# Optimization experiments

Hardware: AMD Instinct MI355X
Metric: run time of the kernel (lower is better)

## Reference

```python
import jax, jax.numpy as jnp
import numpy as np

N, D, C = 4096, 512, 64
MARGIN = 1.0
INF = jnp.float32(1e30)


def setup_inputs() -> dict:
    key = jax.random.key(0)
    k1, k2 = jax.random.split(key)
    embeddings = jax.random.normal(k1, (N, D), dtype=jnp.float32)
    targets = jax.random.randint(k2, (N,), 0, C)
    return {"embeddings": embeddings, "targets": targets}


def _triplet_loss(embeddings, targets, margin=MARGIN):
    # Squared pairwise distances [N, N] (differentiable, used for the loss)
    sq_norms = jnp.sum(embeddings * embeddings, axis=1)
    sq_dist = jnp.maximum(
        sq_norms[:, None] + sq_norms[None, :] - 2.0 * (embeddings @ embeddings.T), 0.0
    )
    # Euclidean distances for mining only (index selection is non-differentiable in torch)
    dist = jnp.sqrt(jax.lax.stop_gradient(sq_dist))

    same = targets[:, None] == targets[None, :]  # [N, N] same-label mask

    # Hardest negative per anchor: argmax_k (d_ap - d_ak + margin) == argmin_k d_ak over negatives
    neg_dist = jnp.where(same, INF, dist)
    n_idx = jnp.argmin(neg_dist, axis=1)   # [N] hardest negative index per anchor
    min_neg = jnp.min(neg_dist, axis=1)    # [N] its euclidean distance

    idx = jnp.arange(dist.shape[0])
    # anchor-positive pairs: same label, a < p (torch.combinations on sorted indices)
    pair_mask = same & (idx[:, None] < idx[None, :])
    # triplet kept only if mined loss (euclidean) strictly positive
    valid = pair_mask & (dist - min_neg[:, None] + margin > 0)

    ap_sq = sq_dist                         # [N, N] squared anchor-positive distances
    an_sq = sq_dist[idx, n_idx]             # [N]   squared anchor-hard-negative distances
    losses = jax.nn.relu(ap_sq - an_sq[:, None] + margin)

    cnt = jnp.sum(valid)
    denom = jnp.maximum(cnt, 1).astype(losses.dtype)
    loss = jnp.sum(jnp.where(valid, losses, 0.0)) / denom

    correct = jnp.sum(valid & (ap_sq < an_sq[:, None]))
    accuracy = correct.astype(jnp.float32) / jnp.maximum(cnt, 1).astype(jnp.float32)
    return loss, accuracy


def reference(embeddings, targets):
    return _triplet_loss(embeddings, targets)
```

## Files before the change

### kernel.cpp

```cpp
#include <hip/hip_runtime.h>

#define N 4096
#define D 512
#define C 64
#define MARGIN 1.0f
#define TILE 128
#define ROWB 128
#define NTILES (N / TILE)
#define NTRI (NTILES * (NTILES + 1) / 2)
#define FINF 3.0e38f
#define MAXM 112
#define SKB 144
#define SLOTW 16
#define LOSS_G 7

typedef __attribute__((ext_vector_type(8))) short short8;
typedef __attribute__((ext_vector_type(4))) float floatx4;

__device__ __forceinline__ unsigned short f2bf(float f) {
  unsigned int u = __float_as_uint(f);
  u += 0x7FFFu + ((u >> 16) & 1u);
  return (unsigned short)(u >> 16);
}

__device__ __forceinline__ void gload_lds16(const void* g, void* l) {
  __builtin_amdgcn_global_load_lds(
      (const __attribute__((address_space(1))) unsigned int*)g,
      (__attribute__((address_space(3))) unsigned int*)l, 16, 0, 0);
}

__global__ __launch_bounds__(256) void prep_kernel(const float* __restrict__ E,
                                                   const int* __restrict__ targets,
                                                   unsigned short* __restrict__ Ebf,
                                                   float* __restrict__ norms,
                                                   unsigned int* __restrict__ an_sq_bits,
                                                   int* __restrict__ cls_mem,
                                                   int* __restrict__ cls_off,
                                                   unsigned int* __restrict__ accs_u,
                                                   unsigned int* __restrict__ done) {
  const int row = blockIdx.x;
  const int tid = threadIdx.x;
  if (row == N) {
    __shared__ unsigned int cnt[C];
    __shared__ unsigned int base[C];
    if (tid == 0) *done = 0u;
    for (int k = tid; k < C * SLOTW; k += 256) accs_u[k] = 0u;
    if (tid < C) cnt[tid] = 0;
    __syncthreads();
    for (int i = tid; i < N; i += 256) atomicAdd(&cnt[targets[i]], 1);
    __syncthreads();
    if (tid == 0) {
      unsigned int s = 0;
      for (int c = 0; c < C; c++) { base[c] = s; s += cnt[c]; }
    }
    __syncthreads();
    if (tid < C) cnt[tid] = base[tid];
    __syncthreads();
    for (int i = tid; i < N; i += 256) {
      const int c = targets[i];
      const unsigned int p = atomicAdd(&cnt[c], 1);
      cls_mem[p] = i;
    }
    if (tid < C) cls_off[tid] = (int)base[tid];
    if (tid == 0) cls_off[C] = N;
    return;
  }
  if (row < 16) an_sq_bits[row * 256 + tid] = 0x7F800000u;
  const float2 v = reinterpret_cast<const float2*>(E + (size_t)row * D)[tid];
  float s = v.x * v.x + v.y * v.y;
  unsigned int packed = ((unsigned int)f2bf(v.y) << 16) | (unsigned int)f2bf(v.x);
  reinterpret_cast<unsigned int*>(Ebf + (size_t)row * D)[tid] = packed;
  for (int off = 32; off > 0; off >>= 1) s += __shfl_down(s, off);
  __shared__ float wsum[4];
  if ((tid & 63) == 0) wsum[tid >> 6] = s;
  __syncthreads();
  if (tid == 0) norms[row] = wsum[0] + wsum[1] + wsum[2] + wsum[3];
}

__global__ __launch_bounds__(256, 3) void gemm_min_kernel(const unsigned short* __restrict__ Ebf,
                                                          const float* __restrict__ norms,
                                                          const int* __restrict__ targets,
                                                          unsigned int* __restrict__ an_sq_bits) {
  const int u = blockIdx.x;
  int i = (int)((sqrtf(8.0f * (float)u + 1.0f) - 1.0f) * 0.5f);
  while ((i + 1) * (i + 2) / 2 <= u) ++i;
  while (i * (i + 1) / 2 > u) --i;
  const int tm = u - i * (i + 1) / 2;
  const int tn = i;

  __shared__ alignas(16) unsigned char As[TILE * ROWB];
  __shared__ alignas(16) unsigned char Bs[TILE * ROWB];
  __shared__ float s_rmin[2][TILE];
  __shared__ float s_cmin[2][TILE];

  const int tid = threadIdx.x;
  const int wave = tid >> 6, lane = tid & 63;
  const int quad = lane >> 4, l16 = lane & 15;
  const int wr = wave >> 1, wc = wave & 1;
  const int rowBase = tm * TILE, colBase = tn * TILE;

  const int lr = lane >> 3;
  const int lq = (lane & 7) ^ lr;
  const int lofs = lr * (D * 2) + lq * 16;
  const unsigned char* gA = (const unsigned char*)Ebf + (size_t)rowBase * (D * 2);
  const unsigned char* gB = (const unsigned char*)Ebf + (size_t)colBase * (D * 2);

  const int swz = l16 & 7;
  int rA[4], rB[4], cq[2];
#pragma unroll
  for (int s = 0; s < 4; s++) {
    rA[s] = (wr * 64 + s * 16 + l16) * ROWB;
    rB[s] = (wc * 64 + s * 16 + l16) * ROWB;
  }
#pragma unroll
  for (int ks = 0; ks < 2; ks++) cq[ks] = ((ks * 4 + quad) ^ swz) * 16;

  floatx4 acc[4][4];
#pragma unroll
  for (int a = 0; a < 4; a++)
#pragma unroll
    for (int b = 0; b < 4; b++) acc[a][b] = (floatx4){0.f, 0.f, 0.f, 0.f};

  for (int k0b = 0; k0b < D * 2; k0b += 128) {
#pragma unroll
    for (int t = 0; t < 4; t++) {
      const int g = wave * 4 + t;
      gload_lds16(gA + (size_t)g * 8 * (D * 2) + lofs + k0b, As + g * 1024);
      gload_lds16(gB + (size_t)g * 8 * (D * 2) + lofs + k0b, Bs + g * 1024);
    }
    __syncthreads();
#pragma unroll
    for (int ks = 0; ks < 2; ks++) {
      short8 af[4], bf[4];
#pragma unroll
      for (int s = 0; s < 4; s++) {
        af[s] = *reinterpret_cast<const short8*>(As + rA[s] + cq[ks]);
        bf[s] = *reinterpret_cast<const short8*>(Bs + rB[s] + cq[ks]);
      }
#pragma unroll
      for (int sm = 0; sm < 4; sm++)
#pragma unroll
        for (int sn = 0; sn < 4; sn++)
          acc[sm][sn] = __builtin_amdgcn_mfma_f32_16x16x32_bf16(af[sm], bf[sn], acc[sm][sn], 0, 0, 0);
    }
    __syncthreads();
  }

  int tcol[4];
  float ncol[4];
#pragma unroll
  for (int sn = 0; sn < 4; sn++) {
    const int gc = colBase + wc * 64 + sn * 16 + l16;
    tcol[sn] = targets[gc];
    ncol[sn] = norms[gc];
  }
  float colmin[4] = {FINF, FINF, FINF, FINF};
#pragma unroll
  for (int sm = 0; sm < 4; sm++) {
#pragma unroll
    for (int r = 0; r < 4; r++) {
      const int rloc = wr * 64 + sm * 16 + quad * 4 + r;
      const int grow = rowBase + rloc;
      const int trow = targets[grow];
      const float nrow = norms[grow];
      float rowmin = FINF;
#pragma unroll
      for (int sn = 0; sn < 4; sn++) {
        const float sq = fmaxf(nrow + ncol[sn] - 2.0f * acc[sm][sn][r], 0.0f);
        if (tcol[sn] != trow) {
          rowmin = fminf(rowmin, sq);
          colmin[sn] = fminf(colmin[sn], sq);
        }
      }
#pragma unroll
      for (int off = 1; off < 16; off <<= 1) rowmin = fminf(rowmin, __shfl_xor(rowmin, off));
      if (l16 == 0) s_rmin[wc][rloc] = rowmin;
    }
  }
#pragma unroll
  for (int sn = 0; sn < 4; sn++) {
    float cm = colmin[sn];
    cm = fminf(cm, __shfl_xor(cm, 16));
    cm = fminf(cm, __shfl_xor(cm, 32));
    if (quad == 0) s_cmin[wr][wc * 64 + sn * 16 + l16] = cm;
  }
  __syncthreads();
  if (tid < TILE) {
    const float m = fminf(s_rmin[0][tid], s_rmin[1][tid]);
    if (m < FINF) atomicMin(&an_sq_bits[rowBase + tid], __float_as_uint(m));
  } else {
    const int c = tid - TILE;
    const float m = fminf(s_cmin[0][c], s_cmin[1][c]);
    if (m < FINF) atomicMin(&an_sq_bits[colBase + c], __float_as_uint(m));
  }
}

__global__ __launch_bounds__(256) void loss_kernel(const unsigned short* __restrict__ Ebf,
                                                   const float* __restrict__ norms,
                                                   const unsigned int* __restrict__ an_sq_bits,
                                                   const int* __restrict__ cls_mem,
                                                   const int* __restrict__ cls_off,
                                                   float* __restrict__ accs,
                                                   unsigned int* __restrict__ done,
                                                   float* __restrict__ out) {
  const int c = blockIdx.x, g = blockIdx.y;
  const int tid = threadIdx.x, wave = tid >> 6, lane = tid & 63;
  const int quad = lane >> 4, l16 = lane & 15;
  const int o = cls_off[c];
  const int s_c = min(cls_off[c + 1] - o, MAXM);
  const int nt = (s_c + 15) >> 4;
  const int npairs = nt * (nt + 1) / 2;
  const bool active = (g * 4 < npairs);

  __shared__ alignas(16) unsigned char S[MAXM * SKB];
  __shared__ int l_mem[MAXM];
  __shared__ float l_norm[MAXM];
  __shared__ float l_an[MAXM];
  __shared__ float s_sum[4];
  __shared__ unsigned int s_cnt[4], s_cor[4];
  __shared__ int s_last;

  if (active) {
    if (tid < s_c) {
      const int m = cls_mem[o + tid];
      l_mem[tid] = m;
      l_norm[tid] = norms[m];
      l_an[tid] = __uint_as_float(an_sq_bits[m]);
    }
    __syncthreads();
    const int p = g * 4 + wave;
    const bool havep = p < npairs;
    int ti = 0, tj = 0;
    if (havep) {
      int pp = p, t = 0;
      while (pp >= nt - t) { pp -= nt - t; t++; }
      ti = t; tj = t + pp;
    }
    floatx4 pacc = (floatx4){0.f, 0.f, 0.f, 0.f};
    for (int k0 = 0; k0 < D; k0 += 64) {
      for (int s = tid; s < s_c * 8; s += 256) {
        const int r = s >> 3, q = s & 7;
        *reinterpret_cast<uint4*>(&S[r * SKB + q * 16]) =
            *reinterpret_cast<const uint4*>(&Ebf[(size_t)l_mem[r] * D + k0 + q * 8]);
      }
      __syncthreads();
      if (havep) {
#pragma unroll
        for (int ks = 0; ks < 2; ks++) {
          const short8 af = *reinterpret_cast<const short8*>(&S[(ti * 16 + l16) * SKB + ks * 64 + quad * 16]);
          const short8 bf = *reinterpret_cast<const short8*>(&S[(tj * 16 + l16) * SKB + ks * 64 + quad * 16]);
          pacc = __builtin_amdgcn_mfma_f32_16x16x32_bf16(af, bf, pacc, 0, 0, 0);
        }
      }
      __syncthreads();
    }

    float bsum = 0.f;
    unsigned int bcnt = 0, bcor = 0;
    if (havep) {
#pragma unroll
      for (int r = 0; r < 4; r++) {
        const int i_loc = ti * 16 + quad * 4 + r;
        const int j_loc = tj * 16 + l16;
        if (i_loc < s_c && j_loc < s_c && (ti < tj || i_loc < j_loc)) {
          const int oi = l_mem[i_loc], oj = l_mem[j_loc];
          const float sq = fmaxf(l_norm[i_loc] + l_norm[j_loc] - 2.0f * pacc[r], 0.0f);
          const float an = (oi < oj) ? l_an[i_loc] : l_an[j_loc];
          if (sqrtf(sq) - sqrtf(an) + MARGIN > 0.0f) {
            bcnt++;
            bsum += fmaxf(sq - an + MARGIN, 0.0f);
            if (sq < an) bcor++;
          }
        }
      }
    }
#pragma unroll
    for (int off = 32; off > 0; off >>= 1) {
      bsum += __shfl_down(bsum, off);
      bcnt += __shfl_down(bcnt, off);
      bcor += __shfl_down(bcor, off);
    }
    if (lane == 0) { s_sum[wave] = bsum; s_cnt[wave] = bcnt; s_cor[wave] = bcor; }
    __syncthreads();
    if (tid == 0) {
      float* slot = accs + (size_t)c * SLOTW;
      atomicAdd(&slot[0], s_sum[0] + s_sum[1] + s_sum[2] + s_sum[3]);
      atomicAdd((unsigned int*)&slot[1], s_cnt[0] + s_cnt[1] + s_cnt[2] + s_cnt[3]);
      atomicAdd((unsigned int*)&slot[2], s_cor[0] + s_cor[1] + s_cor[2] + s_cor[3]);
    }
  }
  __syncthreads();
  if (tid == 0) {
    __threadfence();
    s_last = (atomicAdd(done, 1u) == (unsigned)(C * LOSS_G) - 1u);
  }
  __syncthreads();
  if (s_last) {
    __threadfence();
    if (tid < C) {
      float sum = __uint_as_float(atomicAdd((unsigned int*)&accs[(size_t)tid * SLOTW + 0], 0u));
      unsigned int cnt = atomicAdd((unsigned int*)&accs[(size_t)tid * SLOTW + 1], 0u);
      unsigned int cor = atomicAdd((unsigned int*)&accs[(size_t)tid * SLOTW + 2], 0u);
#pragma unroll
      for (int off = 32; off > 0; off >>= 1) {
        sum += __shfl_down(sum, off);
        cnt += __shfl_down(cnt, off);
        cor += __shfl_down(cor, off);
      }
      if (tid == 0) {
        const float denom = (float)(cnt > 0u ? cnt : 1u);
        out[0] = sum / denom;
        out[1] = (float)cor / denom;
      }
    }
  }
}

extern "C" void kernel_launch(void* const* d_in, const int* in_sizes, int n_in,
                              void* d_out, int out_size, void* d_ws, size_t ws_size,
                              hipStream_t stream) {
  const float* E = (const float*)d_in[0];
  const int* targets = (const int*)d_in[1];
  float* out = (float*)d_out;
  char* ws = (char*)d_ws;
  size_t off = 0;
  unsigned short* Ebf = (unsigned short*)(ws + off); off += (size_t)N * D * 2;
  float* norms = (float*)(ws + off); off += (size_t)N * 4;
  unsigned int* an_sq = (unsigned int*)(ws + off); off += (size_t)N * 4;
  float* accs = (float*)(ws + off); off += (size_t)C * SLOTW * 4;
  int* cls_mem = (int*)(ws + off); off += (size_t)N * 4;
  int* cls_off = (int*)(ws + off); off += 512;
  unsigned int* done = (unsigned int*)(ws + off);

  prep_kernel<<<dim3(N + 1), dim3(256), 0, stream>>>(E, targets, Ebf, norms, an_sq, cls_mem,
                                                     cls_off, (unsigned int*)accs, done);
  gemm_min_kernel<<<dim3(NTRI), dim3(256), 0, stream>>>(Ebf, norms, targets, an_sq);
  loss_kernel<<<dim3(C, LOSS_G), dim3(256), 0, stream>>>(Ebf, norms, an_sq, cls_mem, cls_off,
                                                         accs, done, out);
}
```

Measured before the change: 102.9 us.

## Emit same-class pair distances from GEMM epilogue and drop per-class recompute

```diff
diff --git a/kernel.cpp b/kernel.cpp
--- a/kernel.cpp
+++ b/kernel.cpp
@@ -9,10 +9,9 @@
 #define NTILES (N / TILE)
 #define NTRI (NTILES * (NTILES + 1) / 2)
 #define FINF 3.0e38f
-#define MAXM 112
-#define SKB 144
 #define SLOTW 16
-#define LOSS_G 7
+#define PCAP 1024
+#define LOSSB 128
 
 typedef __attribute__((ext_vector_type(8))) short short8;
 typedef __attribute__((ext_vector_type(4))) float floatx4;
@@ -30,39 +29,16 @@
 }
 
 __global__ __launch_bounds__(256) void prep_kernel(const float* __restrict__ E,
-                                                   const int* __restrict__ targets,
                                                    unsigned short* __restrict__ Ebf,
                                                    float* __restrict__ norms,
                                                    unsigned int* __restrict__ an_sq_bits,
-                                                   int* __restrict__ cls_mem,
-                                                   int* __restrict__ cls_off,
                                                    unsigned int* __restrict__ accs_u,
-                                                   unsigned int* __restrict__ done) {
+                                                   unsigned int* __restrict__ ctrl) {
   const int row = blockIdx.x;
   const int tid = threadIdx.x;
   if (row == N) {
-    __shared__ unsigned int cnt[C];
-    __shared__ unsigned int base[C];
-    if (tid == 0) *done = 0u;
     for (int k = tid; k < C * SLOTW; k += 256) accs_u[k] = 0u;
-    if (tid < C) cnt[tid] = 0;
-    __syncthreads();
-    for (int i = tid; i < N; i += 256) atomicAdd(&cnt[targets[i]], 1);
-    __syncthreads();
-    if (tid == 0) {
-      unsigned int s = 0;
-      for (int c = 0; c < C; c++) { base[c] = s; s += cnt[c]; }
-    }
-    __syncthreads();
-    if (tid < C) cnt[tid] = base[tid];
-    __syncthreads();
-    for (int i = tid; i < N; i += 256) {
-      const int c = targets[i];
-      const unsigned int p = atomicAdd(&cnt[c], 1);
-      cls_mem[p] = i;
-    }
-    if (tid < C) cls_off[tid] = (int)base[tid];
-    if (tid == 0) cls_off[C] = N;
+    if (tid < 2) ctrl[tid] = 0u;
     return;
   }
   if (row < 16) an_sq_bits[row * 256 + tid] = 0x7F800000u;
@@ -80,7 +56,9 @@
 __global__ __launch_bounds__(256, 3) void gemm_min_kernel(const unsigned short* __restrict__ Ebf,
                                                           const float* __restrict__ norms,
                                                           const int* __restrict__ targets,
-                                                          unsigned int* __restrict__ an_sq_bits) {
+                                                          unsigned int* __restrict__ an_sq_bits,
+                                                          uint2* __restrict__ pairs,
+                                                          unsigned int* __restrict__ ctrl) {
   const int u = blockIdx.x;
   int i = (int)((sqrtf(8.0f * (float)u + 1.0f) - 1.0f) * 0.5f);
   while ((i + 1) * (i + 2) / 2 <= u) ++i;
@@ -92,12 +70,16 @@
   __shared__ alignas(16) unsigned char Bs[TILE * ROWB];
   __shared__ float s_rmin[2][TILE];
   __shared__ float s_cmin[2][TILE];
+  __shared__ unsigned int s_pkey[PCAP];
+  __shared__ float s_psq[PCAP];
+  __shared__ unsigned int s_pcnt, s_pbase;
 
   const int tid = threadIdx.x;
   const int wave = tid >> 6, lane = tid & 63;
   const int quad = lane >> 4, l16 = lane & 15;
   const int wr = wave >> 1, wc = wave & 1;
   const int rowBase = tm * TILE, colBase = tn * TILE;
+  if (tid == 0) s_pcnt = 0u;
 
   const int lr = lane >> 3;
   const int lq = (lane & 7) ^ lr;
@@ -146,11 +128,12 @@
     __syncthreads();
   }
 
-  int tcol[4];
+  int tcol[4], gcolv[4];
   float ncol[4];
 #pragma unroll
   for (int sn = 0; sn < 4; sn++) {
     const int gc = colBase + wc * 64 + sn * 16 + l16;
+    gcolv[sn] = gc;
     tcol[sn] = targets[gc];
     ncol[sn] = norms[gc];
   }
@@ -170,6 +153,16 @@
         if (tcol[sn] != trow) {
           rowmin = fminf(rowmin, sq);
           colmin[sn] = fminf(colmin[sn], sq);
+        } else if (grow < gcolv[sn]) {
+          const unsigned int idx = atomicAdd(&s_pcnt, 1u);
+          if (idx < PCAP) {
+            s_pkey[idx] = ((unsigned int)grow << 12) | (unsigned int)gcolv[sn];
+            s_psq[idx] = sq;
+          } else {
+            const unsigned int g = atomicAdd(&ctrl[0], 1u);
+            pairs[g] = make_uint2(((unsigned int)grow << 12) | (unsigned int)gcolv[sn],
+                                  __float_as_uint(sq));
+          }
         }
       }
 #pragma unroll
@@ -193,106 +186,51 @@
     const float m = fminf(s_cmin[0][c], s_cmin[1][c]);
     if (m < FINF) atomicMin(&an_sq_bits[colBase + c], __float_as_uint(m));
   }
-}
-
-__global__ __launch_bounds__(256) void loss_kernel(const unsigned short* __restrict__ Ebf,
-                                                   const float* __restrict__ norms,
+  const unsigned int npair = min(s_pcnt, (unsigned int)PCAP);
+  if (tid == 0) s_pbase = atomicAdd(&ctrl[0], npair);
+  __syncthreads();
+  for (unsigned int r = tid; r < npair; r += 256)
+    pairs[s_pbase + r] = make_uint2(s_pkey[r], __float_as_uint(s_psq[r]));
+}
+
+__global__ __launch_bounds__(256) void loss_kernel(const uint2* __restrict__ pairs,
                                                    const unsigned int* __restrict__ an_sq_bits,
-                                                   const int* __restrict__ cls_mem,
-                                                   const int* __restrict__ cls_off,
                                                    float* __restrict__ accs,
-                                                   unsigned int* __restrict__ done,
+                                                   unsigned int* __restrict__ ctrl,
                                                    float* __restrict__ out) {
-  const int c = blockIdx.x, g = blockIdx.y;
   const int tid = threadIdx.x, wave = tid >> 6, lane = tid & 63;
-  const int quad = lane >> 4, l16 = lane & 15;
-  const int o = cls_off[c];
-  const int s_c = min(cls_off[c + 1] - o, MAXM);
-  const int nt = (s_c + 15) >> 4;
-  const int npairs = nt * (nt + 1) / 2;
-  const bool active = (g * 4 < npairs);
-
-  __shared__ alignas(16) unsigned char S[MAXM * SKB];
-  __shared__ int l_mem[MAXM];
-  __shared__ float l_norm[MAXM];
-  __shared__ float l_an[MAXM];
+  const unsigned int M = ctrl[0];
   __shared__ float s_sum[4];
   __shared__ unsigned int s_cnt[4], s_cor[4];
   __shared__ int s_last;
-
-  if (active) {
-    if (tid < s_c) {
-      const int m = cls_mem[o + tid];
-      l_mem[tid] = m;
-      l_norm[tid] = norms[m];
-      l_an[tid] = __uint_as_float(an_sq_bits[m]);
-    }
-    __syncthreads();
-    const int p = g * 4 + wave;
-    const bool havep = p < npairs;
-    int ti = 0, tj = 0;
-    if (havep) {
-      int pp = p, t = 0;
-      while (pp >= nt - t) { pp -= nt - t; t++; }
-      ti = t; tj = t + pp;
-    }
-    floatx4 pacc = (floatx4){0.f, 0.f, 0.f, 0.f};
-    for (int k0 = 0; k0 < D; k0 += 64) {
-      for (int s = tid; s < s_c * 8; s += 256) {
-        const int r = s >> 3, q = s & 7;
-        *reinterpret_cast<uint4*>(&S[r * SKB + q * 16]) =
-            *reinterpret_cast<const uint4*>(&Ebf[(size_t)l_mem[r] * D + k0 + q * 8]);
-      }
-      __syncthreads();
-      if (havep) {
-#pragma unroll
-        for (int ks = 0; ks < 2; ks++) {
-          const short8 af = *reinterpret_cast<const short8*>(&S[(ti * 16 + l16) * SKB + ks * 64 + quad * 16]);
-          const short8 bf = *reinterpret_cast<const short8*>(&S[(tj * 16 + l16) * SKB + ks * 64 + quad * 16]);
-          pacc = __builtin_amdgcn_mfma_f32_16x16x32_bf16(af, bf, pacc, 0, 0, 0);
-        }
-      }
-      __syncthreads();
-    }
-
-    float bsum = 0.f;
-    unsigned int bcnt = 0, bcor = 0;
-    if (havep) {
-#pragma unroll
-      for (int r = 0; r < 4; r++) {
-        const int i_loc = ti * 16 + quad * 4 + r;
-        const int j_loc = tj * 16 + l16;
-        if (i_loc < s_c && j_loc < s_c && (ti < tj || i_loc < j_loc)) {
-          const int oi = l_mem[i_loc], oj = l_mem[j_loc];
-          const float sq = fmaxf(l_norm[i_loc] + l_norm[j_loc] - 2.0f * pacc[r], 0.0f);
-          const float an = (oi < oj) ? l_an[i_loc] : l_an[j_loc];
-          if (sqrtf(sq) - sqrtf(an) + MARGIN > 0.0f) {
-            bcnt++;
-            bsum += fmaxf(sq - an + MARGIN, 0.0f);
-            if (sq < an) bcor++;
-          }
-        }
-      }
-    }
-#pragma unroll
-    for (int off = 32; off > 0; off >>= 1) {
-      bsum += __shfl_down(bsum, off);
-      bcnt += __shfl_down(bcnt, off);
-      bcor += __shfl_down(bcor, off);
-    }
-    if (lane == 0) { s_sum[wave] = bsum; s_cnt[wave] = bcnt; s_cor[wave] = bcor; }
-    __syncthreads();
-    if (tid == 0) {
-      float* slot = accs + (size_t)c * SLOTW;
-      atomicAdd(&slot[0], s_sum[0] + s_sum[1] + s_sum[2] + s_sum[3]);
-      atomicAdd((unsigned int*)&slot[1], s_cnt[0] + s_cnt[1] + s_cnt[2] + s_cnt[3]);
-      atomicAdd((unsigned int*)&slot[2], s_cor[0] + s_cor[1] + s_cor[2] + s_cor[3]);
-    }
-  }
+  float bsum = 0.f;
+  unsigned int bcnt = 0, bcor = 0;
+  for (unsigned int r = blockIdx.x * 256 + tid; r < M; r += LOSSB * 256) {
+    const uint2 rec = pairs[r];
+    const int a = (int)(rec.x >> 12);
+    const float sq = __uint_as_float(rec.y);
+    const float an = __uint_as_float(an_sq_bits[a]);
+    if (sqrtf(sq) - sqrtf(an) + MARGIN > 0.0f) {
+      bcnt++;
+      bsum += fmaxf(sq - an + MARGIN, 0.0f);
+      if (sq < an) bcor++;
+    }
+  }
+#pragma unroll
+  for (int off = 32; off > 0; off >>= 1) {
+    bsum += __shfl_down(bsum, off);
+    bcnt += __shfl_down(bcnt, off);
+    bcor += __shfl_down(bcor, off);
+  }
+  if (lane == 0) { s_sum[wave] = bsum; s_cnt[wave] = bcnt; s_cor[wave] = bcor; }
   __syncthreads();
   if (tid == 0) {
+    float* slot = accs + (size_t)(blockIdx.x & (C - 1)) * SLOTW;
+    atomicAdd(&slot[0], s_sum[0] + s_sum[1] + s_sum[2] + s_sum[3]);
+    atomicAdd((unsigned int*)&slot[1], s_cnt[0] + s_cnt[1] + s_cnt[2] + s_cnt[3]);
+    atomicAdd((unsigned int*)&slot[2], s_cor[0] + s_cor[1] + s_cor[2] + s_cor[3]);
     __threadfence();
-    s_last = (atomicAdd(done, 1u) == (unsigned)(C * LOSS_G) - 1u);
+    s_last = (atomicAdd(&ctrl[1], 1u) == (unsigned int)LOSSB - 1u);
   }
   __syncthreads();
   if (s_last) {
@@ -328,13 +266,10 @@
   float* norms = (float*)(ws + off); off += (size_t)N * 4;
   unsigned int* an_sq = (unsigned int*)(ws + off); off += (size_t)N * 4;
   float* accs = (float*)(ws + off); off += (size_t)C * SLOTW * 4;
-  int* cls_mem = (int*)(ws + off); off += (size_t)N * 4;
-  int* cls_off = (int*)(ws + off); off += 512;
-  unsigned int* done = (unsigned int*)(ws + off);
-
-  prep_kernel<<<dim3(N + 1), dim3(256), 0, stream>>>(E, targets, Ebf, norms, an_sq, cls_mem,
-                                                     cls_off, (unsigned int*)accs, done);
-  gemm_min_kernel<<<dim3(NTRI), dim3(256), 0, stream>>>(Ebf, norms, targets, an_sq);
-  loss_kernel<<<dim3(C, LOSS_G), dim3(256), 0, stream>>>(Ebf, norms, an_sq, cls_mem, cls_off,
-                                                         accs, done, out);
-}
+  unsigned int* ctrl = (unsigned int*)(ws + off); off += 256;
+  uint2* pairs = (uint2*)(ws + off);
+
+  prep_kernel<<<dim3(N + 1), dim3(256), 0, stream>>>(E, Ebf, norms, an_sq, (unsigned int*)accs, ctrl);
+  gemm_min_kernel<<<dim3(NTRI), dim3(256), 0, stream>>>(Ebf, norms, targets, an_sq, pairs, ctrl);
+  loss_kernel<<<dim3(LOSSB), dim3(256), 0, stream>>>(pairs, an_sq, accs, ctrl, out);
+}
```

Result: faster. 95.93 us (-6.8%).
